# Kernel optimization log

Measured on AMD Instinct MI355X. Metric: run time of the kernel, lower is better.

Reference implementation:

```python
import jax, jax.numpy as jnp
import numpy as np

N = 100000          # buses
E = 200000          # branch edges (avg degree 2, power grid)
IN_DIM = 6          # x[:, 4:10]
EDGE_DIM = 4
HID = 32
OUT_DIM = 2


def _nnconv(x_in, src, dst, edge_attr, w1, b1, w2, b2, root, bias):
    """PyG NNConv (aggr='add', root_weight=True, bias=True)."""
    in_c, out_c = root.shape
    # edge-conditioned weight matrices: [E, in_c, out_c]
    h = jax.nn.relu(edge_attr @ w1 + b1)
    W = (h @ w2 + b2).reshape(-1, in_c, out_c)
    # gather source features, per-edge matvec, scatter-add to targets
    msg = jnp.einsum('ei,eio->eo', x_in[src], W)           # [E, out_c]
    agg = jax.ops.segment_sum(msg, dst, num_segments=x_in.shape[0])
    return agg + x_in @ root + bias


def setup_inputs() -> dict:
    key = jax.random.key(0)
    ks = jax.random.split(key, 8)
    inp = {
        'x': jax.random.normal(ks[0], (N, 10), dtype=jnp.float32),
        'edge_index': jax.random.randint(ks[1], (2, E), 0, N, dtype=jnp.int64),
        'edge_attr': jax.random.normal(ks[2], (E, EDGE_DIM), dtype=jnp.float32),
    }
    dims = [(IN_DIM, HID), (HID, HID), (HID, HID), (HID, OUT_DIM)]
    s = 0.1
    for i, (ic, oc) in enumerate(dims):
        k = jax.random.split(ks[3 + i], 3)
        inp[f'w1_{i}'] = jax.random.normal(k[0], (EDGE_DIM, HID), dtype=jnp.float32) * s
        inp[f'b1_{i}'] = jnp.zeros((HID,), dtype=jnp.float32)
        inp[f'w2_{i}'] = jax.random.normal(k[1], (HID, ic * oc), dtype=jnp.float32) * s
        inp[f'b2_{i}'] = jnp.zeros((ic * oc,), dtype=jnp.float32)
        inp[f'root_{i}'] = jax.random.normal(k[2], (ic, oc), dtype=jnp.float32) * s
        inp[f'bias_{i}'] = jnp.zeros((oc,), dtype=jnp.float32)
    return inp


def reference(x, edge_index, edge_attr,
              w1_0, b1_0, w2_0, b2_0, root_0, bias_0,
              w1_1, b1_1, w2_1, b2_1, root_1, bias_1,
              w1_2, b1_2, w2_2, b2_2, root_2, bias_2,
              w1_3, b1_3, w2_3, b2_3, root_3, bias_3):
    convs = [
        (w1_0, b1_0, w2_0, b2_0, root_0, bias_0),
        (w1_1, b1_1, w2_1, b2_1, root_1, bias_1),
        (w1_2, b1_2, w2_2, b2_2, root_2, bias_2),
        (w1_3, b1_3, w2_3, b2_3, root_3, bias_3),
    ]
    src, dst = edge_index[0], edge_index[1]
    h = x[:, 4:10]                                    # [N, 6]
    n_convs = len(convs)
    for i, p in enumerate(convs):
        h = _nnconv(h, src, dst, edge_attr, *p)
        if i < n_convs - 1:
            h = jax.nn.relu(h)
    return h
```

## Files before the change

kernel.cpp:

```cpp
#include <hip/hip_runtime.h>
#include <hip/hip_fp16.h>

typedef __attribute__((ext_vector_type(2)))  _Float16 half2v;
typedef __attribute__((ext_vector_type(8)))  _Float16 half8v;
typedef __attribute__((ext_vector_type(16))) float    f32x16;

static constexpr int BSWZ_STEPS = 157;
static constexpr int BSWZ_TOT   = BSWZ_STEPS * 512;
static constexpr int W1H_TOT    = 4 * 160;

struct Prm {
    const float* x;
    const float* w1[4]; const float* b1[4];
    const float* w2[4]; const float* b2[4];
    const float* root[4]; const float* bias[4];
    _Float16* xin;
    _Float16* bswz;
    _Float16* w1h;
    _Float16* aggz;
    float* outz;
    int N;
};

__global__ __launch_bounds__(256) void prep(Prm p, int NB8, int NZA, int NZO)
{
    int b = blockIdx.x;
    if (b < 314) {
        int i = b * 256 + threadIdx.x;
        int T = i >> 9, t2 = i & 511;
        int j = t2 & 7, l = (t2 >> 3) & 63;
        int g = l >> 5, o = l & 31;
        int layer, cls, t;
        if (T < 17)       { layer = 0; cls = 0; t = T; }
        else if (T < 19)  { layer = 0; cls = 1; t = T - 17; }
        else if (T < 85)  { layer = 1; cls = 0; t = T - 19; }
        else if (T < 88)  { layer = 1; cls = 1; t = T - 85; }
        else if (T < 154) { layer = 2; cls = 0; t = T - 88; }
        else              { layer = 2; cls = 1; t = T - 154; }
        const int INP   = (layer == 0) ? 8 : 32;
        const int IN_C  = (layer == 0) ? 6 : 32;
        const int OUT_C = 32;
        float v = 0.f;
        if (cls == 0) {
            const int S_MAIN = 2 * INP;
            if (t < S_MAIN) {
                int kap = 16 * t + 8 * g + j;
                int k  = (INP == 8) ? (kap >> 3) : (kap >> 5);
                int ii = (INP == 8) ? (kap & 7)  : (kap & 31);
                if (ii < IN_C)
                    v = p.w2[layer][(size_t)k * (IN_C * OUT_C) + ii * OUT_C + o];
            } else {
                int ii = 16 * (t - S_MAIN) + 8 * g + j;
                if (ii < IN_C)
                    v = p.b2[layer][ii * OUT_C + o];
            }
        } else {
            const int nroot = (layer == 0) ? 1 : 2;
            if (t < nroot) {
                int ii = 16 * t + 8 * g + j;
                if (ii < IN_C)
                    v = p.root[layer][ii * OUT_C + o];
            } else {
                if (g == 0 && j == 0)
                    v = p.bias[layer][o];
            }
        }
        p.bswz[i] = (_Float16)v;
    } else if (b < 314 + NB8) {
        int i = (b - 314) * 256 + threadIdx.x;
        if (i < p.N * 8) {
            int v = i >> 3, c = i & 7;
            float val = (c < 6) ? p.x[(size_t)v * 10 + 4 + c] : 0.f;
            p.xin[i] = (_Float16)val;
        }
    } else if (b < 314 + NB8 + NZA) {
        long long i = (long long)(b - 314 - NB8) * 256 + threadIdx.x;
        if (i < (long long)p.N * 12)
            ((uint4*)p.aggz)[i] = uint4{0u, 0u, 0u, 0u};
    } else if (b < 314 + NB8 + NZA + NZO) {
        int v = (b - 314 - NB8 - NZA) * 256 + threadIdx.x;
        if (v < p.N)
            ((float2*)p.outz)[v] = float2{0.f, 0.f};
    } else {
        for (int i = threadIdx.x; i < W1H_TOT; i += 256) {
            int layer = i / 160, r = i % 160;
            float v = (r < 128) ? p.w1[layer][r]
                                : p.b1[layer][r - 128];
            p.w1h[i] = (_Float16)v;
        }
    }
}

static __device__ __forceinline__ void gather32h(
    const _Float16* __restrict__ fprev, int s, int g, half8v& xh0, half8v& xh1)
{
    const half8v* fp = (const half8v*)(fprev + (size_t)s * 32);
    xh0 = fp[g];
    xh1 = fp[2 + g];
    #pragma unroll
    for (int j = 0; j < 8; ++j) {
        xh0[j] = xh0[j] > (_Float16)0.f ? xh0[j] : (_Float16)0.f;
        xh1[j] = xh1[j] > (_Float16)0.f ? xh1[j] : (_Float16)0.f;
    }
}

static __device__ __forceinline__ half8v splat8(_Float16 h)
{
    half8v r;
    #pragma unroll
    for (int j = 0; j < 8; ++j) r[j] = h;
    return r;
}

static __device__ __forceinline__ void pk_atomic_row(
    _Float16* __restrict__ aggH, int row, int o, float mine)
{
    float oth = __shfl_xor(mine, 1);
    if ((o & 1) == 0 && row >= 0) {
        __half2 v = __floats2half2_rn(mine, oth);
        unsafeAtomicAdd((__half2*)aggH + (((size_t)row << 5) + o) / 2, v);
    }
}

template<int INP>
__global__ __launch_bounds__(1024, 8) void edge(
    const _Float16* __restrict__ xin,
    const _Float16* __restrict__ fprev,
    const int*      __restrict__ src,
    const int*      __restrict__ dst,
    const float*    __restrict__ ea,
    const _Float16* __restrict__ w1h,
    const _Float16* __restrict__ bAll,
    _Float16* __restrict__ aggH,
    int E, int N, int ntileE, int ntot)
{
    constexpr int NREAL = (INP == 32) ? 66 : 17;
    constexpr int NSELF = (INP == 32) ? 3  : 2;
    constexpr int NSTEP = NREAL + NSELF;

    __shared__ half8v ldsb[NSTEP * 64];
    {
        const half8v* bp = (const half8v*)bAll;
        for (int i = threadIdx.x; i < NSTEP * 64; i += 1024)
            ldsb[i] = bp[i];
    }
    __syncthreads();

    const int lane = threadIdx.x & 63;
    const int g = lane >> 5, o = lane & 31;
    const int lrow = lane & 31;
    const int wv = (blockIdx.x * 1024 + threadIdx.x) >> 6;
    const int nw = gridDim.x * 16;

    const half2v* w1p = (const half2v*)w1h;
    const half2v* b1p = (const half2v*)(w1h + 128);
    const half2v zero2 = { (_Float16)0.f, (_Float16)0.f };

    half8v ones;
    #pragma unroll
    for (int j = 0; j < 8; ++j) ones[j] = (_Float16)0.f;
    ones[0] = (_Float16)1.f;

    for (int tile = wv; tile < ntot; tile += nw) {
        f32x16 C;
        #pragma unroll
        for (int i = 0; i < 16; ++i) C[i] = 0.f;

        if (tile < ntileE) {
            const int e0 = tile * 32;
            const int er = e0 + lrow;
            const int ec = er < E ? er : (E - 1);
            const int s  = src[ec];
            const float4 av = *(const float4*)(ea + 4ll * ec);
            half2v eax; eax[0] = (_Float16)av.x; eax[1] = eax[0];
            half2v eay; eay[0] = (_Float16)av.y; eay[1] = eay[0];
            half2v eaz; eaz[0] = (_Float16)av.z; eaz[1] = eaz[0];
            half2v eaw; eaw[0] = (_Float16)av.w; eaw[1] = eaw[0];

            half8v xh0, xh1;
            if constexpr (INP == 32) gather32h(fprev, s, g, xh0, xh1);
            else                     xh0 = *(const half8v*)(xin + (size_t)s * 8);

            if constexpr (INP == 32) {
                #pragma unroll 2
                for (int t = 0; t < 16; ++t) {
                    half2v h2 = eax * w1p[t] + b1p[t];
                    h2 = eay * w1p[16 + t] + h2;
                    h2 = eaz * w1p[32 + t] + h2;
                    h2 = eaw * w1p[48 + t] + h2;
                    h2 = __builtin_elementwise_max(h2, zero2);
                    half8v hsl = splat8(h2[0]);
                    half8v hsh = splat8(h2[1]);
                    half8v bf0 = ldsb[(4*t    ) * 64 + lane];
                    half8v bf1 = ldsb[(4*t + 1) * 64 + lane];
                    half8v bf2 = ldsb[(4*t + 2) * 64 + lane];
                    half8v bf3 = ldsb[(4*t + 3) * 64 + lane];
                    C = __builtin_amdgcn_mfma_f32_32x32x16_f16(hsl * xh0, bf0, C, 0, 0, 0);
                    C = __builtin_amdgcn_mfma_f32_32x32x16_f16(hsl * xh1, bf1, C, 0, 0, 0);
                    C = __builtin_amdgcn_mfma_f32_32x32x16_f16(hsh * xh0, bf2, C, 0, 0, 0);
                    C = __builtin_amdgcn_mfma_f32_32x32x16_f16(hsh * xh1, bf3, C, 0, 0, 0);
                }
                C = __builtin_amdgcn_mfma_f32_32x32x16_f16(xh0, ldsb[64*64 + lane], C, 0, 0, 0);
                C = __builtin_amdgcn_mfma_f32_32x32x16_f16(xh1, ldsb[65*64 + lane], C, 0, 0, 0);
            } else {
                #pragma unroll 4
                for (int t = 0; t < 16; ++t) {
                    half2v h2 = eax * w1p[t] + b1p[t];
                    h2 = eay * w1p[16 + t] + h2;
                    h2 = eaz * w1p[32 + t] + h2;
                    h2 = eaw * w1p[48 + t] + h2;
                    h2 = __builtin_elementwise_max(h2, zero2);
                    half8v hs = splat8(g ? h2[1] : h2[0]);
                    half8v bf = ldsb[t * 64 + lane];
                    C = __builtin_amdgcn_mfma_f32_32x32x16_f16(hs * xh0, bf, C, 0, 0, 0);
                }
                half8v zz;
                #pragma unroll
                for (int j = 0; j < 8; ++j) zz[j] = (_Float16)0.f;
                half8v a = (g == 0) ? xh0 : zz;
                C = __builtin_amdgcn_mfma_f32_32x32x16_f16(a, ldsb[16*64 + lane], C, 0, 0, 0);
            }

            #pragma unroll
            for (int q = 0; q < 4; ++q) {
                const int eb = e0 + 8 * q + 4 * g;
                int rows[4];
                if (eb + 3 < E) {
                    const int4 dd = *(const int4*)(dst + eb);
                    rows[0] = dd.x; rows[1] = dd.y; rows[2] = dd.z; rows[3] = dd.w;
                } else {
                    #pragma unroll
                    for (int m = 0; m < 4; ++m)
                        rows[m] = (eb + m < E) ? dst[eb + m] : -1;
                }
                #pragma unroll
                for (int m = 0; m < 4; ++m)
                    pk_atomic_row(aggH, rows[m], o, C[4*q + m]);
            }
        } else {
            const int v0 = (tile - ntileE) * 32;
            const int vr = v0 + lrow;
            const int vc = vr < N ? vr : (N - 1);

            if constexpr (INP == 32) {
                half8v xh0, xh1;
                gather32h(fprev, vc, g, xh0, xh1);
                C = __builtin_amdgcn_mfma_f32_32x32x16_f16(xh0,  ldsb[(NREAL+0)*64 + lane], C, 0, 0, 0);
                C = __builtin_amdgcn_mfma_f32_32x32x16_f16(xh1,  ldsb[(NREAL+1)*64 + lane], C, 0, 0, 0);
                C = __builtin_amdgcn_mfma_f32_32x32x16_f16(ones, ldsb[(NREAL+2)*64 + lane], C, 0, 0, 0);
            } else {
                half8v xh0 = *(const half8v*)(xin + (size_t)vc * 8);
                C = __builtin_amdgcn_mfma_f32_32x32x16_f16(xh0,  ldsb[(NREAL+0)*64 + lane], C, 0, 0, 0);
                C = __builtin_amdgcn_mfma_f32_32x32x16_f16(ones, ldsb[(NREAL+1)*64 + lane], C, 0, 0, 0);
            }

            #pragma unroll
            for (int q = 0; q < 4; ++q) {
                #pragma unroll
                for (int m = 0; m < 4; ++m) {
                    const int row = v0 + 8*q + 4*g + m;
                    pk_atomic_row(aggH, row < N ? row : -1, o, C[4*q + m]);
                }
            }
        }
    }
}

__global__ __launch_bounds__(256) void l3_fused(
    const _Float16* __restrict__ fprev,
    const int*      __restrict__ src,
    const int*      __restrict__ dst,
    const float*    __restrict__ ea,
    const _Float16* __restrict__ w1h,
    const float*    __restrict__ w2,
    const float*    __restrict__ b2,
    const float*    __restrict__ root,
    const float*    __restrict__ bias,
    float* __restrict__ out, int E, int N)
{
    const int tid = blockIdx.x * 256 + threadIdx.x;

    if (tid < E) {
        const int s = src[tid], d = dst[tid];
        const float4 av = *(const float4*)(ea + 4ll * tid);
        half2v eax; eax[0] = (_Float16)av.x; eax[1] = eax[0];
        half2v eay; eay[0] = (_Float16)av.y; eay[1] = eay[0];
        half2v eaz; eaz[0] = (_Float16)av.z; eaz[1] = eaz[0];
        half2v eaw; eaw[0] = (_Float16)av.w; eaw[1] = eaw[0];

        float xf[32];
        {
            const half8v* fp = (const half8v*)(fprev + (size_t)s * 32);
            #pragma unroll
            for (int q = 0; q < 4; ++q) {
                half8v u = fp[q];
                #pragma unroll
                for (int j = 0; j < 8; ++j)
                    xf[8*q + j] = fmaxf((float)u[j], 0.f);
            }
        }

        const half2v* w1p = (const half2v*)w1h;
        const half2v* b1p = (const half2v*)(w1h + 128);
        const half2v zero2 = { (_Float16)0.f, (_Float16)0.f };

        float m0 = 0.f, m1 = 0.f;
        #pragma unroll 2
        for (int t = 0; t < 16; ++t) {
            half2v h2 = eax * w1p[t] + b1p[t];
            h2 = eay * w1p[16 + t] + h2;
            h2 = eaz * w1p[32 + t] + h2;
            h2 = eaw * w1p[48 + t] + h2;
            h2 = __builtin_elementwise_max(h2, zero2);
            #pragma unroll
            for (int kk = 0; kk < 2; ++kk) {
                const float hk = (float)h2[kk];
                const float* wk = w2 + (size_t)(2*t + kk) * 64;
                float s0 = 0.f, s1 = 0.f;
                #pragma unroll
                for (int i = 0; i < 32; ++i) {
                    s0 = fmaf(xf[i], wk[2*i    ], s0);
                    s1 = fmaf(xf[i], wk[2*i + 1], s1);
                }
                m0 = fmaf(hk, s0, m0);
                m1 = fmaf(hk, s1, m1);
            }
        }
        #pragma unroll
        for (int i = 0; i < 32; ++i) {
            m0 = fmaf(xf[i], b2[2*i    ], m0);
            m1 = fmaf(xf[i], b2[2*i + 1], m1);
        }
        unsafeAtomicAdd(out + 2ll*d,     m0);
        unsafeAtomicAdd(out + 2ll*d + 1, m1);
    } else if (tid < E + N) {
        const int v = tid - E;
        const half8v* fp = (const half8v*)(fprev + (size_t)v * 32);
        float a0 = bias[0], a1 = bias[1];
        #pragma unroll
        for (int q = 0; q < 4; ++q) {
            half8v u = fp[q];
            #pragma unroll
            for (int j = 0; j < 8; ++j) {
                float xi = fmaxf((float)u[j], 0.f);
                a0 = fmaf(xi, root[(8*q + j) * 2    ], a0);
                a1 = fmaf(xi, root[(8*q + j) * 2 + 1], a1);
            }
        }
        unsafeAtomicAdd(out + 2ll*v,     a0);
        unsafeAtomicAdd(out + 2ll*v + 1, a1);
    }
}

extern "C" void kernel_launch(void* const* d_in, const int* in_sizes, int n_in,
                              void* d_out, int out_size, void* d_ws, size_t ws_size,
                              hipStream_t stream)
{
    const float* x  = (const float*)d_in[0];
    const int*   ei = (const int*)d_in[1];
    const float* ea = (const float*)d_in[2];

    const int E = in_sizes[2] / 4;
    const int N = in_sizes[0] / 10;
    const int* src = ei;
    const int* dst = ei + E;

    const float* p[4][6];
    for (int L = 0; L < 4; ++L)
        for (int j = 0; j < 6; ++j)
            p[L][j] = (const float*)d_in[3 + 6 * L + j];

    char* w = (char*)d_ws;
    auto carve = [&](size_t bytes) {
        char* q = w; w += (bytes + 255) & ~(size_t)255; return (void*)q;
    };
    _Float16* xin  = (_Float16*)carve((size_t)N * 8 * 2);
    _Float16* aggz = (_Float16*)carve((size_t)3 * N * 32 * 2);
    _Float16* bswz = (_Float16*)carve((size_t)BSWZ_TOT * 2);
    _Float16* w1hb = (_Float16*)carve((size_t)W1H_TOT * 2);
    _Float16* agg0 = aggz;
    _Float16* agg1 = aggz + (size_t)N * 32;
    _Float16* agg2 = aggz + (size_t)2 * N * 32;
    float* out  = (float*)d_out;

    Prm prm{};
    prm.x = x;
    for (int L = 0; L < 4; ++L) {
        prm.w1[L] = p[L][0]; prm.b1[L] = p[L][1];
        prm.w2[L] = p[L][2]; prm.b2[L] = p[L][3];
        prm.root[L] = p[L][4]; prm.bias[L] = p[L][5];
    }
    prm.xin = xin; prm.bswz = bswz; prm.w1h = w1hb;
    prm.aggz = aggz; prm.outz = out; prm.N = N;

    const int NB8 = (N * 8 + 255) / 256;
    const int NZA = (N * 12 + 255) / 256;
    const int NZO = (N + 255) / 256;

    const int ntileE = (E + 31) / 32;
    const int ntileN = (N + 31) / 32;
    const int ntot   = ntileE + ntileN;
    int NB = (ntot + 15) / 16;
    if (NB > 512) NB = 512;

    const int NB3 = (E + N + 255) / 256;

    prep<<<314 + NB8 + NZA + NZO + 1, 256, 0, stream>>>(prm, NB8, NZA, NZO);

    edge<8><<<NB, 1024, 0, stream>>>(
        xin, nullptr, src, dst, ea, w1hb + 0 * 160,
        bswz + 0 * 512, agg0, E, N, ntileE, ntot);

    edge<32><<<NB, 1024, 0, stream>>>(
        nullptr, agg0, src, dst, ea, w1hb + 1 * 160,
        bswz + 19 * 512, agg1, E, N, ntileE, ntot);

    edge<32><<<NB, 1024, 0, stream>>>(
        nullptr, agg1, src, dst, ea, w1hb + 2 * 160,
        bswz + 88 * 512, agg2, E, N, ntileE, ntot);

    l3_fused<<<NB3, 256, 0, stream>>>(
        agg2, src, dst, ea, w1hb + 3 * 160,
        p[3][2], p[3][3], p[3][4], p[3][5], out, E, N);
}
```

Baseline: 121.0 us.

## Precompute per-node layer-3 projections, reducing per-edge work to a 32-term dot

The last layer now runs in two kernels. A node kernel computes, once per node, x·W2[k] for all 32 hidden units plus x·b2, stores them as fp16 in a 72-half buffer, and writes the root/bias term directly into the output instead of adding it atomically. An edge kernel then gathers that precomputed row by source, evaluates the edge MLP hidden layer, and takes a 32-term dot product before scatter-adding. This replaces the per-edge 32x32x2 contraction with a per-node one (E=2N), at the cost of an extra launch, a 144-byte per-node intermediate, and fp16 rounding of the projections. The prep kernel also fills layer-3 swizzled weights that the new code does not appear to read.

```diff
diff --git a/kernel.cpp b/kernel.cpp
--- a/kernel.cpp
+++ b/kernel.cpp
@@ -5,7 +5,7 @@
 typedef __attribute__((ext_vector_type(8)))  _Float16 half8v;
 typedef __attribute__((ext_vector_type(16))) float    f32x16;
 
-static constexpr int BSWZ_STEPS = 157;
+static constexpr int BSWZ_STEPS = 226;
 static constexpr int BSWZ_TOT   = BSWZ_STEPS * 512;
 static constexpr int W1H_TOT    = 4 * 160;
 
@@ -25,7 +25,7 @@
 __global__ __launch_bounds__(256) void prep(Prm p, int NB8, int NZA, int NZO)
 {
     int b = blockIdx.x;
-    if (b < 314) {
+    if (b < 452) {
         int i = b * 256 + threadIdx.x;
         int T = i >> 9, t2 = i & 511;
         int j = t2 & 7, l = (t2 >> 3) & 63;
@@ -36,10 +36,12 @@
         else if (T < 85)  { layer = 1; cls = 0; t = T - 19; }
         else if (T < 88)  { layer = 1; cls = 1; t = T - 85; }
         else if (T < 154) { layer = 2; cls = 0; t = T - 88; }
-        else              { layer = 2; cls = 1; t = T - 154; }
+        else if (T < 157) { layer = 2; cls = 1; t = T - 154; }
+        else if (T < 223) { layer = 3; cls = 0; t = T - 157; }
+        else              { layer = 3; cls = 1; t = T - 223; }
         const int INP   = (layer == 0) ? 8 : 32;
         const int IN_C  = (layer == 0) ? 6 : 32;
-        const int OUT_C = 32;
+        const int OUT_C = (layer == 3) ? 2 : 32;
         float v = 0.f;
         if (cls == 0) {
             const int S_MAIN = 2 * INP;
@@ -47,38 +49,38 @@
                 int kap = 16 * t + 8 * g + j;
                 int k  = (INP == 8) ? (kap >> 3) : (kap >> 5);
                 int ii = (INP == 8) ? (kap & 7)  : (kap & 31);
-                if (ii < IN_C)
+                if (ii < IN_C && o < OUT_C)
                     v = p.w2[layer][(size_t)k * (IN_C * OUT_C) + ii * OUT_C + o];
             } else {
                 int ii = 16 * (t - S_MAIN) + 8 * g + j;
-                if (ii < IN_C)
+                if (ii < IN_C && o < OUT_C)
                     v = p.b2[layer][ii * OUT_C + o];
             }
         } else {
             const int nroot = (layer == 0) ? 1 : 2;
             if (t < nroot) {
                 int ii = 16 * t + 8 * g + j;
-                if (ii < IN_C)
+                if (ii < IN_C && o < OUT_C)
                     v = p.root[layer][ii * OUT_C + o];
             } else {
-                if (g == 0 && j == 0)
+                if (g == 0 && j == 0 && o < OUT_C)
                     v = p.bias[layer][o];
             }
         }
         p.bswz[i] = (_Float16)v;
-    } else if (b < 314 + NB8) {
-        int i = (b - 314) * 256 + threadIdx.x;
+    } else if (b < 452 + NB8) {
+        int i = (b - 452) * 256 + threadIdx.x;
         if (i < p.N * 8) {
             int v = i >> 3, c = i & 7;
             float val = (c < 6) ? p.x[(size_t)v * 10 + 4 + c] : 0.f;
             p.xin[i] = (_Float16)val;
         }
-    } else if (b < 314 + NB8 + NZA) {
-        long long i = (long long)(b - 314 - NB8) * 256 + threadIdx.x;
+    } else if (b < 452 + NB8 + NZA) {
+        long long i = (long long)(b - 452 - NB8) * 256 + threadIdx.x;
         if (i < (long long)p.N * 12)
             ((uint4*)p.aggz)[i] = uint4{0u, 0u, 0u, 0u};
-    } else if (b < 314 + NB8 + NZA + NZO) {
-        int v = (b - 314 - NB8 - NZA) * 256 + threadIdx.x;
+    } else if (b < 452 + NB8 + NZA + NZO) {
+        int v = (b - 452 - NB8 - NZA) * 256 + threadIdx.x;
         if (v < p.N)
             ((float2*)p.outz)[v] = float2{0.f, 0.f};
     } else {
@@ -266,90 +268,115 @@
     }
 }
 
-__global__ __launch_bounds__(256) void l3_fused(
+__global__ __launch_bounds__(256) void l3_pre(
     const _Float16* __restrict__ fprev,
+    const float* __restrict__ w2,
+    const float* __restrict__ b2,
+    const float* __restrict__ root,
+    const float* __restrict__ bias,
+    _Float16* __restrict__ P,
+    float* __restrict__ out, int N)
+{
+    int v = blockIdx.x * 256 + threadIdx.x;
+    if (v >= N) return;
+
+    float xf[32];
+    {
+        const half8v* fp = (const half8v*)(fprev + (size_t)v * 32);
+        #pragma unroll
+        for (int q = 0; q < 4; ++q) {
+            half8v u = fp[q];
+            #pragma unroll
+            for (int j = 0; j < 8; ++j)
+                xf[8*q + j] = fmaxf((float)u[j], 0.f);
+        }
+    }
+
+    union { uint4 u[9]; half2v h[36]; } pb;
+    #pragma unroll
+    for (int k = 0; k < 32; ++k) {
+        const float* wk = w2 + (size_t)k * 64;
+        float p0 = 0.f, p1 = 0.f;
+        #pragma unroll
+        for (int i = 0; i < 32; ++i) {
+            p0 = fmaf(xf[i], wk[2*i    ], p0);
+            p1 = fmaf(xf[i], wk[2*i + 1], p1);
+        }
+        half2v hp; hp[0] = (_Float16)p0; hp[1] = (_Float16)p1;
+        pb.h[k] = hp;
+    }
+    {
+        float q0 = 0.f, q1 = 0.f;
+        #pragma unroll
+        for (int i = 0; i < 32; ++i) {
+            q0 = fmaf(xf[i], b2[2*i    ], q0);
+            q1 = fmaf(xf[i], b2[2*i + 1], q1);
+        }
+        half2v hq; hq[0] = (_Float16)q0; hq[1] = (_Float16)q1;
+        pb.h[32] = hq;
+        half2v hz; hz[0] = (_Float16)0.f; hz[1] = (_Float16)0.f;
+        pb.h[33] = hz; pb.h[34] = hz; pb.h[35] = hz;
+    }
+    uint4* dp = (uint4*)(P + (size_t)v * 72);
+    #pragma unroll
+    for (int q = 0; q < 9; ++q) dp[q] = pb.u[q];
+
+    float a0 = bias[0], a1 = bias[1];
+    #pragma unroll
+    for (int i = 0; i < 32; ++i) {
+        a0 = fmaf(xf[i], root[2*i    ], a0);
+        a1 = fmaf(xf[i], root[2*i + 1], a1);
+    }
+    float2 o2; o2.x = a0; o2.y = a1;
+    ((float2*)out)[v] = o2;
+}
+
+__global__ __launch_bounds__(256) void l3_edge(
     const int*      __restrict__ src,
     const int*      __restrict__ dst,
     const float*    __restrict__ ea,
     const _Float16* __restrict__ w1h,
-    const float*    __restrict__ w2,
-    const float*    __restrict__ b2,
-    const float*    __restrict__ root,
-    const float*    __restrict__ bias,
-    float* __restrict__ out, int E, int N)
-{
-    const int tid = blockIdx.x * 256 + threadIdx.x;
-
-    if (tid < E) {
-        const int s = src[tid], d = dst[tid];
-        const float4 av = *(const float4*)(ea + 4ll * tid);
-        half2v eax; eax[0] = (_Float16)av.x; eax[1] = eax[0];
-        half2v eay; eay[0] = (_Float16)av.y; eay[1] = eay[0];
-        half2v eaz; eaz[0] = (_Float16)av.z; eaz[1] = eaz[0];
-        half2v eaw; eaw[0] = (_Float16)av.w; eaw[1] = eaw[0];
-
-        float xf[32];
-        {
-            const half8v* fp = (const half8v*)(fprev + (size_t)s * 32);
-            #pragma unroll
-            for (int q = 0; q < 4; ++q) {
-                half8v u = fp[q];
-                #pragma unroll
-                for (int j = 0; j < 8; ++j)
-                    xf[8*q + j] = fmaxf((float)u[j], 0.f);
-            }
-        }
-
-        const half2v* w1p = (const half2v*)w1h;
-        const half2v* b1p = (const half2v*)(w1h + 128);
-        const half2v zero2 = { (_Float16)0.f, (_Float16)0.f };
-
-        float m0 = 0.f, m1 = 0.f;
-        #pragma unroll 2
-        for (int t = 0; t < 16; ++t) {
-            half2v h2 = eax * w1p[t] + b1p[t];
-            h2 = eay * w1p[16 + t] + h2;
-            h2 = eaz * w1p[32 + t] + h2;
-            h2 = eaw * w1p[48 + t] + h2;
-            h2 = __builtin_elementwise_max(h2, zero2);
-            #pragma unroll
-            for (int kk = 0; kk < 2; ++kk) {
-                const float hk = (float)h2[kk];
-                const float* wk = w2 + (size_t)(2*t + kk) * 64;
-                float s0 = 0.f, s1 = 0.f;
-                #pragma unroll
-                for (int i = 0; i < 32; ++i) {
-                    s0 = fmaf(xf[i], wk[2*i    ], s0);
-                    s1 = fmaf(xf[i], wk[2*i + 1], s1);
-                }
-                m0 = fmaf(hk, s0, m0);
-                m1 = fmaf(hk, s1, m1);
-            }
-        }
+    const _Float16* __restrict__ P,
+    float* __restrict__ out, int E)
+{
+    int e = blockIdx.x * 256 + threadIdx.x;
+    if (e >= E) return;
+
+    const int s = src[e], d = dst[e];
+    const float4 av = *(const float4*)(ea + 4ll * e);
+    half2v eax; eax[0] = (_Float16)av.x; eax[1] = eax[0];
+    half2v eay; eay[0] = (_Float16)av.y; eay[1] = eay[0];
+    half2v eaz; eaz[0] = (_Float16)av.z; eaz[1] = eaz[0];
+    half2v eaw; eaw[0] = (_Float16)av.w; eaw[1] = eaw[0];
+
+    union { uint4 u[9]; half2v h[36]; } pr;
+    {
+        const uint4* pp = (const uint4*)(P + (size_t)s * 72);
         #pragma unroll
-        for (int i = 0; i < 32; ++i) {
-            m0 = fmaf(xf[i], b2[2*i    ], m0);
-            m1 = fmaf(xf[i], b2[2*i + 1], m1);
-        }
-        unsafeAtomicAdd(out + 2ll*d,     m0);
-        unsafeAtomicAdd(out + 2ll*d + 1, m1);
-    } else if (tid < E + N) {
-        const int v = tid - E;
-        const half8v* fp = (const half8v*)(fprev + (size_t)v * 32);
-        float a0 = bias[0], a1 = bias[1];
-        #pragma unroll
-        for (int q = 0; q < 4; ++q) {
-            half8v u = fp[q];
-            #pragma unroll
-            for (int j = 0; j < 8; ++j) {
-                float xi = fmaxf((float)u[j], 0.f);
-                a0 = fmaf(xi, root[(8*q + j) * 2    ], a0);
-                a1 = fmaf(xi, root[(8*q + j) * 2 + 1], a1);
-            }
-        }
-        unsafeAtomicAdd(out + 2ll*v,     a0);
-        unsafeAtomicAdd(out + 2ll*v + 1, a1);
-    }
+        for (int q = 0; q < 9; ++q) pr.u[q] = pp[q];
+    }
+
+    const half2v* w1p = (const half2v*)w1h;
+    const half2v* b1p = (const half2v*)(w1h + 128);
+    const half2v zero2 = { (_Float16)0.f, (_Float16)0.f };
+
+    float m0 = (float)pr.h[32][0];
+    float m1 = (float)pr.h[32][1];
+    #pragma unroll 4
+    for (int t = 0; t < 16; ++t) {
+        half2v h2 = eax * w1p[t] + b1p[t];
+        h2 = eay * w1p[16 + t] + h2;
+        h2 = eaz * w1p[32 + t] + h2;
+        h2 = eaw * w1p[48 + t] + h2;
+        h2 = __builtin_elementwise_max(h2, zero2);
+        const float h0 = (float)h2[0], h1 = (float)h2[1];
+        m0 = fmaf(h0, (float)pr.h[2*t    ][0], m0);
+        m1 = fmaf(h0, (float)pr.h[2*t    ][1], m1);
+        m0 = fmaf(h1, (float)pr.h[2*t + 1][0], m0);
+        m1 = fmaf(h1, (float)pr.h[2*t + 1][1], m1);
+    }
+    unsafeAtomicAdd(out + 2ll*d,     m0);
+    unsafeAtomicAdd(out + 2ll*d + 1, m1);
 }
 
 extern "C" void kernel_launch(void* const* d_in, const int* in_sizes, int n_in,
@@ -378,6 +405,7 @@
     _Float16* aggz = (_Float16*)carve((size_t)3 * N * 32 * 2);
     _Float16* bswz = (_Float16*)carve((size_t)BSWZ_TOT * 2);
     _Float16* w1hb = (_Float16*)carve((size_t)W1H_TOT * 2);
+    _Float16* Pbuf = (_Float16*)carve((size_t)N * 72 * 2);
     _Float16* agg0 = aggz;
     _Float16* agg1 = aggz + (size_t)N * 32;
     _Float16* agg2 = aggz + (size_t)2 * N * 32;
@@ -403,9 +431,10 @@
     int NB = (ntot + 15) / 16;
     if (NB > 512) NB = 512;
 
-    const int NB3 = (E + N + 255) / 256;
-
-    prep<<<314 + NB8 + NZA + NZO + 1, 256, 0, stream>>>(prm, NB8, NZA, NZO);
+    const int NBN = (N + 255) / 256;
+    const int NBE = (E + 255) / 256;
+
+    prep<<<452 + NB8 + NZA + NZO + 1, 256, 0, stream>>>(prm, NB8, NZA, NZO);
 
     edge<8><<<NB, 1024, 0, stream>>>(
         xin, nullptr, src, dst, ea, w1hb + 0 * 160,
@@ -419,7 +448,9 @@
         nullptr, agg1, src, dst, ea, w1hb + 2 * 160,
         bswz + 88 * 512, agg2, E, N, ntileE, ntot);
 
-    l3_fused<<<NB3, 256, 0, stream>>>(
-        agg2, src, dst, ea, w1hb + 3 * 160,
-        p[3][2], p[3][3], p[3][4], p[3][5], out, E, N);
-}
+    l3_pre<<<NBN, 256, 0, stream>>>(
+        agg2, p[3][2], p[3][3], p[3][4], p[3][5], Pbuf, out, N);
+
+    l3_edge<<<NBE, 256, 0, stream>>>(
+        src, dst, ea, w1hb + 3 * 160, Pbuf, out, E);
+}
```

After: 152.5 us (median of 3 runs). +26.1%, slower.
